# Kernel optimization log

Hardware: AMD Instinct MI355X
Metric: run time of the kernel (lower is better)

## Reference

```python
import jax, jax.numpy as jnp
import numpy as np


def _binop(ei, ej):
    # diagonal linear recurrence combine: (a_i, b_i) * (a_j, b_j) -> (a_j*a_i, a_j*b_i + b_j)
    ai, bi = ei
    aj, bj = ej
    return aj * ai, aj * bi + bj


def setup_inputs() -> dict:
    key = jax.random.key(0)
    ks = jax.random.split(key, 9)
    B_, T, D_in, D_out, N = 16, 2048, 512, 512, 512
    inp = {
        "input": jax.random.normal(ks[0], (B_, T, D_in), dtype=jnp.float32),
        "D": jax.random.normal(ks[1], (D_out, D_in), dtype=jnp.float32) / np.sqrt(D_in),
        "nu_log": jax.random.normal(ks[2], (N,), dtype=jnp.float32),
        "theta_log": jax.random.normal(ks[3], (N,), dtype=jnp.float32),
        "gamma_log": jax.random.normal(ks[4], (N,), dtype=jnp.float32),
        "B_re": jax.random.normal(ks[5], (N, D_in), dtype=jnp.float32) / np.sqrt(2 * D_in),
        "B_im": jax.random.normal(ks[6], (N, D_in), dtype=jnp.float32) / np.sqrt(2 * D_in),
        "C_re": jax.random.normal(ks[7], (D_out, N), dtype=jnp.float32) / np.sqrt(N),
        "C_im": jax.random.normal(ks[8], (D_out, N), dtype=jnp.float32) / np.sqrt(N),
    }
    return inp


def reference(input, D, nu_log, theta_log, gamma_log, B_re, B_im, C_re, C_im):
    # ss_params
    lam_abs = jnp.exp(-jnp.exp(nu_log))                      # [N]
    lam_phase = jnp.exp(theta_log)                           # [N]
    lam = lam_abs * (jnp.cos(lam_phase) + 1j * jnp.sin(lam_phase))  # complex [N]
    gamma = jnp.exp(gamma_log)                               # [N]
    Bc = (B_re + 1j * B_im) * gamma[:, None]                 # [N, D_in]
    Cc = C_re + 1j * C_im                                    # [D_out, N]

    # input projection: Bu_elements [batch, T, N] (complex)
    Bu = input.astype(Bc.dtype) @ Bc.T
    lam_el = jnp.broadcast_to(lam, Bu.shape)

    # parallel associative scan over time axis (initial state is zero)
    _, states = jax.lax.associative_scan(_binop, (lam_el, Bu), axis=1)

    # readout
    y = jnp.real(states @ Cc.T) + input @ D.T                # [batch, T, D_out]
    return y
```

## Files before the change

### kernel.cpp

```cpp
#include <hip/hip_runtime.h>
#include <hip/hip_fp16.h>

typedef _Float16 f16;
typedef __attribute__((ext_vector_type(8))) _Float16 f16x8;
typedef __attribute__((ext_vector_type(4))) _Float16 f16x4;
typedef __attribute__((ext_vector_type(2))) _Float16 f16x2;
typedef __attribute__((ext_vector_type(4))) float f32x4;

#define B_SZ 16
#define T_SZ 2048
#define DIN 512
#define DOUT 512
#define N_SZ 512
#define M_SZ (B_SZ * T_SZ)
#define LCHUNK 64
#define NCHUNK 32

__device__ __forceinline__ void gload_lds16(const void* g, void* l) {
  __builtin_amdgcn_global_load_lds(
      (const __attribute__((address_space(1))) void*)g,
      (__attribute__((address_space(3))) void*)l, 16, 0, 0);
}


__global__ void prep_all(const float* __restrict__ nu_log,
                         const float* __restrict__ theta_log,
                         const float* __restrict__ gamma_log,
                         const float* __restrict__ B_re, const float* __restrict__ B_im,
                         const float* __restrict__ C_re, const float* __restrict__ C_im,
                         const float* __restrict__ Dm, const float* __restrict__ input,
                         float2* __restrict__ lam2, float2* __restrict__ lamL2,
                         float2* __restrict__ lamp,
                         f16* __restrict__ W1, f16* __restrict__ W2,
                         f16* __restrict__ A2) {
  int b = blockIdx.x;
  if (b < 2) {
    int n = b * 256 + threadIdx.x;
    float nu = expf(nu_log[n]);
    float ph = expf(theta_log[n]);
    float la = expf(-nu);
    lam2[n] = make_float2(la * cosf(ph), la * sinf(ph));
    float laL = expf(-nu * (float)LCHUNK);
    float phL = ph * (float)LCHUNK;
    lamL2[n] = make_float2(laL * cosf(phL), laL * sinf(phL));
  } else if (b < 4) {
    int n = (b - 2) * 256 + threadIdx.x;
    float nu = expf(nu_log[n]);
    float ph = expf(theta_log[n]);
    float la = expf(-nu);
    float2 l1 = make_float2(la * cosf(ph), la * sinf(ph));
    float2 cur = l1;
    for (int j = 0; j < LCHUNK; ++j) {
      lamp[(size_t)j * 512 + n] = cur;
      float nre = cur.x * l1.x - cur.y * l1.y;
      cur.y = cur.x * l1.y + cur.y * l1.x;
      cur.x = nre;
    }
  } else if (b < 4 + 2048) {
    int tid = (b - 4) * 256 + threadIdx.x;
    int np = tid >> 9;
    int d = tid & 511;
    int n = np >> 1;
    float g = expf(gamma_log[n]);
    const float* src = (np & 1) ? B_im : B_re;
    W1[(size_t)np * 512 + d] = (f16)(src[(size_t)n * 512 + d] * g);
  } else if (b < 4 + 2048 + 3072) {
    int tid = (b - 2052) * 256 + threadIdx.x;
    int j = tid / 1536;
    int k = tid - j * 1536;
    float v;
    if (k < 512)       v =  C_re[(size_t)j * 512 + k];
    else if (k < 1024) v = -C_im[(size_t)j * 512 + (k - 512)];
    else               v =  Dm[(size_t)j * 512 + (k - 1024)];
    W2[(size_t)j * 1536 + k] = (f16)v;
  } else {
    int tid = (b - 5124) * 256 + threadIdx.x;
    int m = tid >> 6;
    int d0 = (tid & 63) << 3;
    const float4* p = (const float4*)(input + (size_t)m * DIN + d0);
    float4 a = p[0], c = p[1];
    f16x8 h;
    h[0] = (f16)a.x; h[1] = (f16)a.y; h[2] = (f16)a.z; h[3] = (f16)a.w;
    h[4] = (f16)c.x; h[5] = (f16)c.y; h[6] = (f16)c.z; h[7] = (f16)c.w;
    *(f16x8*)(A2 + (size_t)m * 1536 + 1024 + d0) = h;
  }
}


__global__ void scan_b(const float2* __restrict__ S, const float2* __restrict__ lamL2,
                       float2* __restrict__ Carry) {
  int tid = blockIdx.x * 256 + threadIdx.x;
  int n = tid & 511;
  int b = tid >> 9;
  float2 lL = lamL2[n];
  float cre = 0.f, cim = 0.f;
  for (int c = 0; c < NCHUNK; ++c) {
    size_t idx = (size_t)(b * NCHUNK + c) * 512 + n;
    Carry[idx] = make_float2(cre, cim);
    float2 s = S[idx];
    float nre = lL.x * cre - lL.y * cim + s.x;
    cim = lL.x * cim + lL.y * cre + s.y;
    cre = nre;
  }
}

__global__ void apply_carry(const unsigned* __restrict__ sloc,
                            const float2* __restrict__ lamp,
                            const float2* __restrict__ Carry,
                            f16* __restrict__ A2) {
  int tid = blockIdx.x * 256 + threadIdx.x;
  int g = tid & 127;
  int m = tid >> 7;
  int j = m & 63;
  int bc = m >> 6;
  int n0 = g * 4;
  const float2* lpp = lamp + (size_t)j * 512 + n0;
  const float2* crp = Carry + (size_t)bc * 512 + n0;
  uint4 sv = *(const uint4*)(sloc + (size_t)m * 512 + n0);
  unsigned u4[4] = {sv.x, sv.y, sv.z, sv.w};
  f16x4 ore, oim;
#pragma unroll
  for (int q = 0; q < 4; ++q) {
    f16x2 u = __builtin_bit_cast(f16x2, u4[q]);
    float2 lp = lpp[q];
    float2 cr = crp[q];
    ore[q] = (f16)((float)u.x + lp.x * cr.x - lp.y * cr.y);
    oim[q] = (f16)((float)u.y + lp.x * cr.y + lp.y * cr.x);
  }
  *(f16x4*)(A2 + (size_t)m * 1536 + n0) = ore;
  *(f16x4*)(A2 + (size_t)m * 1536 + 512 + n0) = oim;
}


template <typename CT, bool FUSE>
__global__ __launch_bounds__(512, 2) void gemm256(
    const f16* __restrict__ A, int lda,
    const f16* __restrict__ Bm, int ldb,
    CT* __restrict__ C, int ldc, int K, int nxt,
    const float2* __restrict__ lam2, unsigned* __restrict__ sloc,
    float2* __restrict__ Svec) {
  extern __shared__ f16 smem[];
  f16* sA = smem;
  f16* sB = smem + 2 * 16384;

  const int tid = threadIdx.x;
  const int lane = tid & 63;
  const int wid = tid >> 6;
  const int wr = wid >> 2;
  const int wc = wid & 3;
  const int fr = lane & 15;
  const int fg = lane >> 4;
  const int xr = fr & 7;

  const int nwg = gridDim.x;
  const int id = blockIdx.x;
  const int swz = (id & 7) * (nwg >> 3) + (id >> 3);
  const int m0 = (swz / nxt) * 256;
  const int n0 = (swz % nxt) * 256;

  const int srow = tid >> 3;
  const int scol = ((tid & 7) ^ (srow & 7)) * 8;
  const int sdst = wid * 512;

  const int NT = K >> 6;

  f32x4 acc[8][4];
#pragma unroll
  for (int i = 0; i < 8; ++i)
#pragma unroll
    for (int j = 0; j < 4; ++j) acc[i][j] = f32x4{0.f, 0.f, 0.f, 0.f};

  const int ar0 = wr * 128;
  const int bc0 = wc * 64;

  auto stage = [&](int t) {
    const int b = t & 1;
    f16* dA = sA + b * 16384 + sdst;
    f16* dB = sB + b * 16384 + sdst;
    const f16* gA = A + (size_t)(m0 + srow) * lda + t * 64 + scol;
    const f16* gB = Bm + (size_t)(n0 + srow) * ldb + t * 64 + scol;
    gload_lds16(gA, dA);
    gload_lds16(gA + (size_t)64 * lda, dA + 4096);
    gload_lds16(gA + (size_t)128 * lda, dA + 8192);
    gload_lds16(gA + (size_t)192 * lda, dA + 12288);
    gload_lds16(gB, dB);
    gload_lds16(gB + (size_t)64 * ldb, dB + 4096);
    gload_lds16(gB + (size_t)128 * ldb, dB + 8192);
    gload_lds16(gB + (size_t)192 * ldb, dB + 12288);
  };

  auto barrier = [&]() {
    __builtin_amdgcn_sched_barrier(0);
    __builtin_amdgcn_s_barrier();
    __builtin_amdgcn_sched_barrier(0);
  };

  stage(0);
  asm volatile("s_waitcnt vmcnt(0)" ::: "memory");
  barrier();

  f16x8 bf[4][2];
  for (int t = 0; t < NT; ++t) {
    const int b = t & 1;
    const f16* bA = sA + b * 16384;
    const f16* bB = sB + b * 16384;
    if (t + 1 < NT) stage(t + 1);
#pragma unroll
    for (int h = 0; h < 4; ++h) {
      if (h == 0) {
#pragma unroll
        for (int nrep = 0; nrep < 4; ++nrep)
#pragma unroll
          for (int ks = 0; ks < 2; ++ks) {
            int row = bc0 + nrep * 16 + fr;
            bf[nrep][ks] =
                *(const f16x8*)(bB + row * 64 + (((ks * 4 + fg) ^ xr) * 8));
          }
      }
      f16x8 af[2][2];
#pragma unroll
      for (int mi = 0; mi < 2; ++mi)
#pragma unroll
        for (int ks = 0; ks < 2; ++ks) {
          int row = ar0 + (h * 2 + mi) * 16 + fr;
          af[mi][ks] =
              *(const f16x8*)(bA + row * 64 + (((ks * 4 + fg) ^ xr) * 8));
        }
      __builtin_amdgcn_s_setprio(1);
#pragma unroll
      for (int mi = 0; mi < 2; ++mi)
#pragma unroll
        for (int nrep = 0; nrep < 4; ++nrep)
#pragma unroll
          for (int ks = 0; ks < 2; ++ks)
            acc[h * 2 + mi][nrep] = __builtin_amdgcn_mfma_f32_16x16x32_f16(
                af[mi][ks], bf[nrep][ks], acc[h * 2 + mi][nrep], 0, 0, 0);
      __builtin_amdgcn_s_setprio(0);
      if (h == 3 && t + 1 < NT)
        asm volatile("s_waitcnt vmcnt(0)" ::: "memory");
      barrier();
    }
  }

  if constexpr (FUSE) {
    f16* reg = smem + wid * 8192;
#pragma unroll
    for (int mi = 0; mi < 8; ++mi)
#pragma unroll
      for (int ni = 0; ni < 4; ++ni)
#pragma unroll
        for (int r = 0; r < 4; ++r)
          reg[(mi * 16 + fg * 4 + r) * 64 + ni * 16 + fr] = (f16)acc[mi][ni][r];
    __syncthreads();
    const int half = lane >> 5;
    const int nc = lane & 31;
    const int n = ((n0 + wc * 64) >> 1) + nc;
    const float2 l2 = lam2[n];
    const f16* col = smem + wid * 8192 + (half * 64) * 64 + 2 * nc;
    const int mbase = m0 + wr * 128 + half * 64;
    unsigned* sp = sloc + (size_t)mbase * 512 + n;
    float sre = 0.f, sim = 0.f;
#pragma unroll 1
    for (int j0 = 0; j0 < 64; j0 += 8) {
      f16x2 u[8];
#pragma unroll
      for (int q = 0; q < 8; ++q) u[q] = *(const f16x2*)(col + (j0 + q) * 64);
#pragma unroll
      for (int q = 0; q < 8; ++q) {
        float nre = l2.x * sre - l2.y * sim + (float)u[q].x;
        sim = l2.x * sim + l2.y * sre + (float)u[q].y;
        sre = nre;
        f16x2 o;
        o.x = (f16)sre;
        o.y = (f16)sim;
        sp[(size_t)(j0 + q) * 512] = __builtin_bit_cast(unsigned, o);
      }
    }
    Svec[(size_t)((m0 >> 11) * NCHUNK + ((mbase >> 6) & (NCHUNK - 1))) * 512 + n] =
        make_float2(sre, sim);
  } else {
#pragma unroll
    for (int mi = 0; mi < 8; ++mi) {
      int rbase = m0 + ar0 + mi * 16 + fg * 4;
#pragma unroll
      for (int ni = 0; ni < 4; ++ni) {
        int col = n0 + bc0 + ni * 16 + fr;
#pragma unroll
        for (int r = 0; r < 4; ++r)
          C[(size_t)(rbase + r) * ldc + col] = (CT)acc[mi][ni][r];
      }
    }
  }
}


extern "C" void kernel_launch(void* const* d_in, const int* in_sizes, int n_in,
                              void* d_out, int out_size, void* d_ws, size_t ws_size,
                              hipStream_t stream) {
  const float* input = (const float*)d_in[0];
  const float* Dmat = (const float*)d_in[1];
  const float* nu_log = (const float*)d_in[2];
  const float* theta_log = (const float*)d_in[3];
  const float* gamma_log = (const float*)d_in[4];
  const float* B_re = (const float*)d_in[5];
  const float* B_im = (const float*)d_in[6];
  const float* C_re = (const float*)d_in[7];
  const float* C_im = (const float*)d_in[8];
  float* y = (float*)d_out;

  char* ws = (char*)d_ws;
  size_t off = 0;
  auto alloc = [&](size_t bytes) {
    void* p = ws + off;
    off = (off + bytes + 255) & ~(size_t)255;
    return p;
  };
  float2* lam2 = (float2*)alloc(N_SZ * sizeof(float2));
  float2* lamL2 = (float2*)alloc(N_SZ * sizeof(float2));
  float2* lamp = (float2*)alloc((size_t)LCHUNK * N_SZ * sizeof(float2));
  f16* W1 = (f16*)alloc((size_t)2 * N_SZ * DIN * 2);
  f16* W2 = (f16*)alloc((size_t)DOUT * 1536 * 2);
  f16* A2 = (f16*)alloc((size_t)M_SZ * 1536 * 2);
  unsigned* sloc = (unsigned*)alloc((size_t)M_SZ * N_SZ * 4);
  float2* S = (float2*)alloc((size_t)B_SZ * NCHUNK * N_SZ * sizeof(float2));
  float2* Carry = (float2*)alloc((size_t)B_SZ * NCHUNK * N_SZ * sizeof(float2));

  const int shmem = 131072;
  {
    auto* g1 = gemm256<f16, true>;
    auto* g2 = gemm256<float, false>;
    hipFuncSetAttribute((const void*)g1,
                        hipFuncAttributeMaxDynamicSharedMemorySize, shmem);
    hipFuncSetAttribute((const void*)g2,
                        hipFuncAttributeMaxDynamicSharedMemorySize, shmem);
  }

  prep_all<<<13316, 256, 0, stream>>>(nu_log, theta_log, gamma_log, B_re, B_im,
                                      C_re, C_im, Dmat, input, lam2, lamL2, lamp,
                                      W1, W2, A2);

  gemm256<f16, true><<<512, 512, shmem, stream>>>(
      A2 + 1024, 1536, W1, 512, (f16*)nullptr, 0, 512, 4, lam2, sloc, S);

  scan_b<<<(B_SZ * N_SZ) / 256, 256, 0, stream>>>(S, lamL2, Carry);

  apply_carry<<<(M_SZ * 128) / 256, 256, 0, stream>>>(sloc, lamp, Carry, A2);

  gemm256<float, false><<<256, 512, shmem, stream>>>(
      A2, 1536, W2, 1536, y, 512, 1536, 2, nullptr, nullptr, nullptr);
}
```

Measured before the change: 154.3 us.

## Fuse carry application into output GEMM A-operand staging

Removes the separate apply_carry kernel. The final GEMM now builds its first 1024 K-columns on the fly, loading the local scan states plus lambda powers and chunk carries into registers, combining them, and writing f16 tiles straight into LDS. The interleaved re/im layout is matched by reordering the W2 columns. This avoids writing and rereading the large A2 state buffer. In exchange the GEMM's A staging for those K-tiles uses register loads and ALU work instead of asynchronous global-to-LDS copies, which may stall the pipeline and raise register pressure.

```diff
diff --git a/kernel.cpp b/kernel.cpp
--- a/kernel.cpp
+++ b/kernel.cpp
@@ -3,7 +3,6 @@
 
 typedef _Float16 f16;
 typedef __attribute__((ext_vector_type(8))) _Float16 f16x8;
-typedef __attribute__((ext_vector_type(4))) _Float16 f16x4;
 typedef __attribute__((ext_vector_type(2))) _Float16 f16x2;
 typedef __attribute__((ext_vector_type(4))) float f32x4;
 
@@ -32,7 +31,7 @@
                          float2* __restrict__ lam2, float2* __restrict__ lamL2,
                          float2* __restrict__ lamp,
                          f16* __restrict__ W1, f16* __restrict__ W2,
-                         f16* __restrict__ A2) {
+                         f16* __restrict__ inp16) {
   int b = blockIdx.x;
   if (b < 2) {
     int n = b * 256 + threadIdx.x;
@@ -69,9 +68,12 @@
     int j = tid / 1536;
     int k = tid - j * 1536;
     float v;
-    if (k < 512)       v =  C_re[(size_t)j * 512 + k];
-    else if (k < 1024) v = -C_im[(size_t)j * 512 + (k - 512)];
-    else               v =  Dm[(size_t)j * 512 + (k - 1024)];
+    if (k < 1024) {
+      int n = k >> 1;
+      v = (k & 1) ? -C_im[(size_t)j * 512 + n] : C_re[(size_t)j * 512 + n];
+    } else {
+      v = Dm[(size_t)j * 512 + (k - 1024)];
+    }
     W2[(size_t)j * 1536 + k] = (f16)v;
   } else {
     int tid = (b - 5124) * 256 + threadIdx.x;
@@ -82,7 +84,7 @@
     f16x8 h;
     h[0] = (f16)a.x; h[1] = (f16)a.y; h[2] = (f16)a.z; h[3] = (f16)a.w;
     h[4] = (f16)c.x; h[5] = (f16)c.y; h[6] = (f16)c.z; h[7] = (f16)c.w;
-    *(f16x8*)(A2 + (size_t)m * 1536 + 1024 + d0) = h;
+    *(f16x8*)(inp16 + (size_t)m * 512 + d0) = h;
   }
 }
 
@@ -104,41 +106,16 @@
   }
 }
 
-__global__ void apply_carry(const unsigned* __restrict__ sloc,
-                            const float2* __restrict__ lamp,
-                            const float2* __restrict__ Carry,
-                            f16* __restrict__ A2) {
-  int tid = blockIdx.x * 256 + threadIdx.x;
-  int g = tid & 127;
-  int m = tid >> 7;
-  int j = m & 63;
-  int bc = m >> 6;
-  int n0 = g * 4;
-  const float2* lpp = lamp + (size_t)j * 512 + n0;
-  const float2* crp = Carry + (size_t)bc * 512 + n0;
-  uint4 sv = *(const uint4*)(sloc + (size_t)m * 512 + n0);
-  unsigned u4[4] = {sv.x, sv.y, sv.z, sv.w};
-  f16x4 ore, oim;
-#pragma unroll
-  for (int q = 0; q < 4; ++q) {
-    f16x2 u = __builtin_bit_cast(f16x2, u4[q]);
-    float2 lp = lpp[q];
-    float2 cr = crp[q];
-    ore[q] = (f16)((float)u.x + lp.x * cr.x - lp.y * cr.y);
-    oim[q] = (f16)((float)u.y + lp.x * cr.y + lp.y * cr.x);
-  }
-  *(f16x4*)(A2 + (size_t)m * 1536 + n0) = ore;
-  *(f16x4*)(A2 + (size_t)m * 1536 + 512 + n0) = oim;
-}
-
-
-template <typename CT, bool FUSE>
+
+template <typename CT, bool FUSE, bool CARRY>
 __global__ __launch_bounds__(512, 2) void gemm256(
     const f16* __restrict__ A, int lda,
     const f16* __restrict__ Bm, int ldb,
     CT* __restrict__ C, int ldc, int K, int nxt,
-    const float2* __restrict__ lam2, unsigned* __restrict__ sloc,
-    float2* __restrict__ Svec) {
+    const float2* __restrict__ lam2, unsigned* __restrict__ sloc_out,
+    float2* __restrict__ Svec,
+    const unsigned* __restrict__ sloc_in, const float2* __restrict__ lamp,
+    const float2* __restrict__ Carry) {
   extern __shared__ f16 smem[];
   f16* sA = smem;
   f16* sB = smem + 2 * 16384;
@@ -173,20 +150,66 @@
   const int ar0 = wr * 128;
   const int bc0 = wc * 64;
 
-  auto stage = [&](int t) {
-    const int b = t & 1;
-    f16* dA = sA + b * 16384 + sdst;
-    f16* dB = sB + b * 16384 + sdst;
-    const f16* gA = A + (size_t)(m0 + srow) * lda + t * 64 + scol;
+  auto stageB = [&](int t) {
+    f16* dB = sB + (t & 1) * 16384 + sdst;
     const f16* gB = Bm + (size_t)(n0 + srow) * ldb + t * 64 + scol;
+    gload_lds16(gB, dB);
+    gload_lds16(gB + (size_t)64 * ldb, dB + 4096);
+    gload_lds16(gB + (size_t)128 * ldb, dB + 8192);
+    gload_lds16(gB + (size_t)192 * ldb, dB + 12288);
+  };
+  auto stageA_g = [&](int t) {
+    f16* dA = sA + (t & 1) * 16384 + sdst;
+    const int kc = CARRY ? (t - 16) * 64 : t * 64;
+    const f16* gA = A + (size_t)(m0 + srow) * lda + kc + scol;
     gload_lds16(gA, dA);
     gload_lds16(gA + (size_t)64 * lda, dA + 4096);
     gload_lds16(gA + (size_t)128 * lda, dA + 8192);
     gload_lds16(gA + (size_t)192 * lda, dA + 12288);
-    gload_lds16(gB, dB);
-    gload_lds16(gB + (size_t)64 * ldb, dB + 4096);
-    gload_lds16(gB + (size_t)128 * ldb, dB + 8192);
-    gload_lds16(gB + (size_t)192 * ldb, dB + 12288);
+  };
+
+  uint4 sl[4];
+  float2 lpq[4];
+  float2 crq[4][4];
+
+  auto cstage_issue = [&](int t) {
+    const int nq0 = t * 32 + (scol >> 1);
+    const unsigned* sp = sloc_in + (size_t)(m0 + srow) * 512 + nq0;
+    const float2* lpp = lamp + (size_t)srow * 512 + nq0;
+    const float2* crp = Carry + (size_t)(m0 >> 6) * 512 + nq0;
+#pragma unroll
+    for (int q = 0; q < 4; ++q) lpq[q] = lpp[q];
+#pragma unroll
+    for (int i = 0; i < 4; ++i) {
+      sl[i] = *(const uint4*)(sp + (size_t)i * 64 * 512);
+#pragma unroll
+      for (int q = 0; q < 4; ++q) crq[i][q] = crp[(size_t)i * 512 + q];
+    }
+  };
+  auto cstage_finish = [&](int t) {
+    f16* dst = sA + (t & 1) * 16384 + tid * 8;
+#pragma unroll
+    for (int i = 0; i < 4; ++i) {
+      unsigned u4[4] = {sl[i].x, sl[i].y, sl[i].z, sl[i].w};
+      f16x8 o;
+#pragma unroll
+      for (int q = 0; q < 4; ++q) {
+        f16x2 u = __builtin_bit_cast(f16x2, u4[q]);
+        float lx = lpq[q].x, ly = lpq[q].y;
+        float cx = crq[i][q].x, cy = crq[i][q].y;
+        o[2 * q] = (f16)((float)u.x + lx * cx - ly * cy);
+        o[2 * q + 1] = (f16)((float)u.y + lx * cy + ly * cx);
+      }
+      *(f16x8*)(dst + i * 4096) = o;
+    }
+  };
+
+  auto stage_issue = [&](int t) {
+    stageB(t);
+    if (CARRY && t < 16)
+      cstage_issue(t);
+    else
+      stageA_g(t);
   };
 
   auto barrier = [&]() {
@@ -195,8 +218,13 @@
     __builtin_amdgcn_sched_barrier(0);
   };
 
-  stage(0);
-  asm volatile("s_waitcnt vmcnt(0)" ::: "memory");
+  stage_issue(0);
+  if (CARRY) {
+    cstage_finish(0);
+    asm volatile("s_waitcnt vmcnt(0) lgkmcnt(0)" ::: "memory");
+  } else {
+    asm volatile("s_waitcnt vmcnt(0)" ::: "memory");
+  }
   barrier();
 
   f16x8 bf[4][2];
@@ -204,7 +232,7 @@
     const int b = t & 1;
     const f16* bA = sA + b * 16384;
     const f16* bB = sB + b * 16384;
-    if (t + 1 < NT) stage(t + 1);
+    if (t + 1 < NT) stage_issue(t + 1);
 #pragma unroll
     for (int h = 0; h < 4; ++h) {
       if (h == 0) {
@@ -236,8 +264,14 @@
             acc[h * 2 + mi][nrep] = __builtin_amdgcn_mfma_f32_16x16x32_f16(
                 af[mi][ks], bf[nrep][ks], acc[h * 2 + mi][nrep], 0, 0, 0);
       __builtin_amdgcn_s_setprio(0);
-      if (h == 3 && t + 1 < NT)
-        asm volatile("s_waitcnt vmcnt(0)" ::: "memory");
+      if (h == 3 && t + 1 < NT) {
+        if (CARRY && t + 1 < 16) {
+          cstage_finish(t + 1);
+          asm volatile("s_waitcnt vmcnt(0) lgkmcnt(0)" ::: "memory");
+        } else {
+          asm volatile("s_waitcnt vmcnt(0)" ::: "memory");
+        }
+      }
       barrier();
     }
   }
@@ -258,7 +292,7 @@
     const float2 l2 = lam2[n];
     const f16* col = smem + wid * 8192 + (half * 64) * 64 + 2 * nc;
     const int mbase = m0 + wr * 128 + half * 64;
-    unsigned* sp = sloc + (size_t)mbase * 512 + n;
+    unsigned* sp = sloc_out + (size_t)mbase * 512 + n;
     float sre = 0.f, sim = 0.f;
 #pragma unroll 1
     for (int j0 = 0; j0 < 64; j0 += 8) {
@@ -320,15 +354,15 @@
   float2* lamp = (float2*)alloc((size_t)LCHUNK * N_SZ * sizeof(float2));
   f16* W1 = (f16*)alloc((size_t)2 * N_SZ * DIN * 2);
   f16* W2 = (f16*)alloc((size_t)DOUT * 1536 * 2);
-  f16* A2 = (f16*)alloc((size_t)M_SZ * 1536 * 2);
+  f16* inp16 = (f16*)alloc((size_t)M_SZ * DIN * 2);
   unsigned* sloc = (unsigned*)alloc((size_t)M_SZ * N_SZ * 4);
   float2* S = (float2*)alloc((size_t)B_SZ * NCHUNK * N_SZ * sizeof(float2));
   float2* Carry = (float2*)alloc((size_t)B_SZ * NCHUNK * N_SZ * sizeof(float2));
 
   const int shmem = 131072;
   {
-    auto* g1 = gemm256<f16, true>;
-    auto* g2 = gemm256<float, false>;
+    auto* g1 = gemm256<f16, true, false>;
+    auto* g2 = gemm256<float, false, true>;
     hipFuncSetAttribute((const void*)g1,
                         hipFuncAttributeMaxDynamicSharedMemorySize, shmem);
     hipFuncSetAttribute((const void*)g2,
@@ -337,15 +371,15 @@
 
   prep_all<<<13316, 256, 0, stream>>>(nu_log, theta_log, gamma_log, B_re, B_im,
                                       C_re, C_im, Dmat, input, lam2, lamL2, lamp,
-                                      W1, W2, A2);
-
-  gemm256<f16, true><<<512, 512, shmem, stream>>>(
-      A2 + 1024, 1536, W1, 512, (f16*)nullptr, 0, 512, 4, lam2, sloc, S);
+                                      W1, W2, inp16);
+
+  gemm256<f16, true, false><<<512, 512, shmem, stream>>>(
+      inp16, 512, W1, 512, (f16*)nullptr, 0, 512, 4, lam2, sloc, S,
+      nullptr, nullptr, nullptr);
 
   scan_b<<<(B_SZ * N_SZ) / 256, 256, 0, stream>>>(S, lamL2, Carry);
 
-  apply_carry<<<(M_SZ * 128) / 256, 256, 0, stream>>>(sloc, lamp, Carry, A2);
-
-  gemm256<float, false><<<256, 512, shmem, stream>>>(
-      A2, 1536, W2, 1536, y, 512, 1536, 2, nullptr, nullptr, nullptr);
-}
+  gemm256<float, false, true><<<256, 512, shmem, stream>>>(
+      inp16, 512, W2, 1536, y, 512, 1536, 2, nullptr, nullptr, nullptr,
+      sloc, lamp, Carry);
+}
```

Result: faster. 141.8 us (-8.1%).
